# Performance work log

Hardware: AMD Instinct MI355X
Metric: run time of the kernel (lower is better)

Reference implementation:

```python
import jax, jax.numpy as jnp
import numpy as np

LN_EPS = 1e-5


def setup_inputs() -> dict:
    key = jax.random.key(0)
    k1, k2, k3, k4 = jax.random.split(key, 4)
    B, S, H, NH = 32, 256, 4096, 16
    scale = (2.0 ** 0.5) * ((3.0 / H) ** 0.5)
    inp = jax.random.normal(k1, (B, S, H), dtype=jnp.float32)
    mask = jax.random.randint(k2, (B, S), 0, 2, dtype=jnp.int32)  # 1 = padded key
    weight = jnp.ones((H,), dtype=jnp.float32)
    bias = jnp.zeros((H,), dtype=jnp.float32)
    qkv = jax.random.normal(k3, (H, 3 * H), dtype=jnp.float32) * scale
    o = jax.random.normal(k4, (H, H), dtype=jnp.float32) * scale
    return {"inp": inp, "mask": mask, "weight": weight, "bias": bias,
            "qkv": qkv, "o": o, "isPre": 1}


def _layer_norm(x, weight, bias):
    mu = jnp.mean(x, axis=-1, keepdims=True)
    var = jnp.mean(jnp.square(x - mu), axis=-1, keepdims=True)
    return (x - mu) * jax.lax.rsqrt(var + LN_EPS) * weight + bias


def _mha(x, mask, weight, bias, qkv, o, isPre, head_num=16):
    B, S, H = x.shape
    D = H // head_num
    xn = _layer_norm(x, weight, bias) if isPre else x
    # fused QKV projection: [B,S,3H]
    proj = jnp.einsum('bsh,hk->bsk', xn, qkv)
    q, k, v = jnp.split(proj, 3, axis=-1)
    q = q.reshape(B, S, head_num, D)
    k = k.reshape(B, S, head_num, D)
    v = v.reshape(B, S, head_num, D)
    scores = jnp.einsum('bqnd,bknd->bnqk', q, k) / jnp.sqrt(jnp.float32(D))
    # mask[b,k]==1 -> key k is padding, exclude from softmax
    neg = jnp.finfo(scores.dtype).min
    scores = jnp.where(mask[:, None, None, :] != 0, neg, scores)
    attn = jax.nn.softmax(scores, axis=-1)
    ctx = jnp.einsum('bnqk,bknd->bqnd', attn, v).reshape(B, S, H)
    out = jnp.einsum('bsh,ho->bso', ctx, o)
    if not isPre:
        out = _layer_norm(out, weight, bias)
    return out


def reference(inp, mask, weight, bias, qkv, o, isPre):
    return _mha(inp, mask, weight, bias, qkv, o, bool(isPre))
```

## Files before the change

kernel.cpp:

```cpp
#include <hip/hip_runtime.h>
#include <stdint.h>

typedef unsigned short u16;
typedef short bf16x8 __attribute__((ext_vector_type(8)));
typedef float f32x4 __attribute__((ext_vector_type(4)));

#define MFMA16(a, b, c) __builtin_amdgcn_mfma_f32_16x16x32_bf16((a), (b), (c), 0, 0, 0)

#define GLOAD_LDS16(gp, lp)                                                        \
  __builtin_amdgcn_global_load_lds((const __attribute__((address_space(1))) void*)(gp), \
                                   (__attribute__((address_space(3))) void*)(lp), 16, 0, 0)

#define BARRIER asm volatile("s_barrier" ::: "memory")
#define WAITV(n) asm volatile("s_waitcnt vmcnt(" #n ")" ::: "memory")

__device__ __forceinline__ u16 f2bf(float x) {
  union { float f; uint32_t u; } v; v.f = x;
  uint32_t r = (v.u + 0x7FFFu + ((v.u >> 16) & 1u)) >> 16;
  return (u16)r;
}

__global__ __launch_bounds__(256) void transpose_bf16(const float* __restrict__ in,
                                                      u16* __restrict__ out, int R, int C) {
  __shared__ float tile[32][33];
  int nCt = C >> 5;
  int bid = blockIdx.x;
  int r0 = (bid / nCt) << 5, c0 = (bid % nCt) << 5;
  int t = threadIdx.x;
  int r = t >> 3, cc = (t & 7) << 2;
  float4 v = *reinterpret_cast<const float4*>(in + (size_t)(r0 + r) * C + c0 + cc);
  tile[r][cc] = v.x; tile[r][cc + 1] = v.y; tile[r][cc + 2] = v.z; tile[r][cc + 3] = v.w;
  __syncthreads();
  int c = t >> 3, rr = (t & 7) << 2;
  ushort4 u;
  u.x = f2bf(tile[rr][c]);     u.y = f2bf(tile[rr + 1][c]);
  u.z = f2bf(tile[rr + 2][c]); u.w = f2bf(tile[rr + 3][c]);
  *reinterpret_cast<ushort4*>(out + (size_t)(c0 + c) * R + r0 + rr) = u;
}

__global__ __launch_bounds__(256) void ln_bf16(const float* __restrict__ in,
                                               const float* __restrict__ w,
                                               const float* __restrict__ bia,
                                               u16* __restrict__ out) {
  int row = blockIdx.x, t = threadIdx.x;
  const float* x = in + (size_t)row * 4096;
  float4 v[4];
  float s = 0.f, sq = 0.f;
#pragma unroll
  for (int i = 0; i < 4; i++) {
    v[i] = *reinterpret_cast<const float4*>(x + i * 1024 + t * 4);
    s  += v[i].x + v[i].y + v[i].z + v[i].w;
    sq += v[i].x * v[i].x + v[i].y * v[i].y + v[i].z * v[i].z + v[i].w * v[i].w;
  }
#pragma unroll
  for (int off = 32; off > 0; off >>= 1) { s += __shfl_down(s, off); sq += __shfl_down(sq, off); }
  __shared__ float red[8];
  int wid = t >> 6, lane = t & 63;
  if (lane == 0) { red[wid] = s; red[4 + wid] = sq; }
  __syncthreads();
  if (t == 0) {
    float st = red[0] + red[1] + red[2] + red[3];
    float sqt = red[4] + red[5] + red[6] + red[7];
    float mu = st * (1.f / 4096.f);
    float var = sqt * (1.f / 4096.f) - mu * mu;
    red[0] = mu; red[1] = rsqrtf(var + 1e-5f);
  }
  __syncthreads();
  float mu = red[0], rs = red[1];
#pragma unroll
  for (int i = 0; i < 4; i++) {
    float4 wv = *reinterpret_cast<const float4*>(w + i * 1024 + t * 4);
    float4 bv = *reinterpret_cast<const float4*>(bia + i * 1024 + t * 4);
    ushort4 u;
    u.x = f2bf((v[i].x - mu) * rs * wv.x + bv.x);
    u.y = f2bf((v[i].y - mu) * rs * wv.y + bv.y);
    u.z = f2bf((v[i].z - mu) * rs * wv.z + bv.z);
    u.w = f2bf((v[i].w - mu) * rs * wv.w + bv.w);
    *reinterpret_cast<ushort4*>(out + (size_t)row * 4096 + i * 1024 + t * 4) = u;
  }
}


#define LDA8(AR, Ab, mh) do {                                                     \
  _Pragma("unroll")                                                               \
  for (int mf = 0; mf < 4; mf++) {                                                \
    int lr = (mh)*128 + wm64 + mf*16 + llo;                                       \
    const char* rb = (Ab) + lr*128;                                               \
    int sw = (lr & 7) << 4;                                                       \
    AR[mf*2+0] = *reinterpret_cast<const bf16x8*>(rb + ((lhi16) ^ sw));           \
    AR[mf*2+1] = *reinterpret_cast<const bf16x8*>(rb + ((64 + lhi16) ^ sw));      \
  }                                                                               \
} while (0)

#define LDB4(BR, Bb, nh) do {                                                     \
  _Pragma("unroll")                                                               \
  for (int nf = 0; nf < 2; nf++) {                                                \
    int lr = (nh)*128 + wn32 + nf*16 + llo;                                       \
    const char* rb = (Bb) + lr*128;                                               \
    int sw = (lr & 7) << 4;                                                       \
    BR[nf*2+0] = *reinterpret_cast<const bf16x8*>(rb + ((lhi16) ^ sw));           \
    BR[nf*2+1] = *reinterpret_cast<const bf16x8*>(rb + ((64 + lhi16) ^ sw));      \
  }                                                                               \
} while (0)

#define MMAQ(AR, BR, mh, nh) do {                                                 \
  __builtin_amdgcn_s_setprio(1);                                                  \
  _Pragma("unroll")                                                               \
  for (int mf = 0; mf < 4; mf++)                                                  \
    _Pragma("unroll")                                                             \
    for (int nf = 0; nf < 2; nf++) {                                              \
      acc[(mh)*4+mf][(nh)*2+nf] = MFMA16(AR[mf*2+0], BR[nf*2+0], acc[(mh)*4+mf][(nh)*2+nf]); \
      acc[(mh)*4+mf][(nh)*2+nf] = MFMA16(AR[mf*2+1], BR[nf*2+1], acc[(mh)*4+mf][(nh)*2+nf]); \
    }                                                                             \
  __builtin_amdgcn_s_setprio(0);                                                  \
} while (0)

#define STAGE(isB, h, cbuf, ktile) do {                                           \
  const u16* g_ = (isB) ? Bt : A;                                                 \
  int base0_ = (isB) ? n0 : m0;                                                   \
  char* lb_ = smc + (cbuf)*65536 + (isB)*32768 + (h)*16384;                       \
  _Pragma("unroll")                                                               \
  for (int i_ = 0; i_ < 2; i_++) {                                                \
    int L_ = i_*512 + t;                                                          \
    int lr_ = (h)*128 + (L_ >> 3);                                                \
    int sl_ = (L_ & 7) ^ (lr_ & 7);                                               \
    int r_ = (isB) ? (((lr_ & 128) >> 2) | ((lr_ & 96) << 1) | (lr_ & 31))        \
                   : ((lr_ & 63) | ((lr_ & 64) << 1) | ((lr_ & 128) >> 1));       \
    GLOAD_LDS16(g_ + (size_t)(base0_ + r_) * K + (ktile)*64 + sl_*8, lb_ + L_*16);\
  }                                                                               \
} while (0)

template <int EPI>
__global__ __launch_bounds__(512, 2) void gemm256(const u16* __restrict__ A, const u16* __restrict__ Bt,
                                                  void* __restrict__ Cout, u16* __restrict__ vT,
                                                  int M, int N, int K, int nbn) {
  __shared__ u16 sm[65536];
  char* smc = (char*)sm;
  int bid = blockIdx.x;
  int s = bid >> 8, local = bid & 255;
  int xcd = local & 7, j = local >> 3;
  int trow = ((xcd >> 1) << 2) + (j >> 3);
  int tcol = ((xcd & 1) << 3) + (j & 7);
  int nsc = nbn >> 4;
  int sr = s / nsc, sc = s - sr * nsc;
  int tm = (sr << 4) + trow, tn = (sc << 4) + tcol;
  int m0 = tm << 8, n0 = tn << 8;
  int t = threadIdx.x;
  int w = t >> 6, lane = t & 63;
  int wm = w >> 2, wn = w & 3;
  int llo = lane & 15, lhi = lane >> 4;
  int wm64 = wm << 6, wn32 = wn << 5, lhi16 = lhi << 4;
  f32x4 acc[8][4] = {};
  bf16x8 aR[8], b0R[4], b1R[4];
  int NT = K >> 6;
  STAGE(0, 0, 0, 0); STAGE(1, 0, 0, 0); STAGE(1, 1, 0, 0); STAGE(0, 1, 0, 0);
  WAITV(4); BARRIER;
#pragma unroll 1
  for (int kt = 0; kt < NT - 1; kt++) {
    int c = kt & 1, cn = c ^ 1;
    const char* Ab = smc + c * 65536;
    const char* Bb = Ab + 32768;
    LDA8(aR, Ab, 0); LDB4(b0R, Bb, 0);
    STAGE(0, 0, cn, kt + 1);
    BARRIER;
    MMAQ(aR, b0R, 0, 0);
    WAITV(4); BARRIER;
    LDB4(b1R, Bb, 1);
    STAGE(1, 0, cn, kt + 1);
    BARRIER;
    MMAQ(aR, b1R, 0, 1);
    WAITV(4); BARRIER;
    LDA8(aR, Ab, 1);
    STAGE(1, 1, cn, kt + 1);
    BARRIER;
    MMAQ(aR, b1R, 1, 1);
    BARRIER;
    STAGE(0, 1, cn, kt + 1);
    BARRIER;
    MMAQ(aR, b0R, 1, 0);
    WAITV(4); BARRIER;
  }
  {
    int c = (NT - 1) & 1;
    const char* Ab = smc + c * 65536;
    const char* Bb = Ab + 32768;
    LDA8(aR, Ab, 0); LDB4(b0R, Bb, 0);
    MMAQ(aR, b0R, 0, 0);
    WAITV(2); BARRIER;
    LDB4(b1R, Bb, 1);
    MMAQ(aR, b1R, 0, 1);
    WAITV(0); BARRIER;
    LDA8(aR, Ab, 1);
    MMAQ(aR, b1R, 1, 1);
    MMAQ(aR, b0R, 1, 0);
  }
  if (EPI == 2) {
    float* C = (float*)Cout;
#pragma unroll
    for (int mi = 0; mi < 8; mi++)
#pragma unroll
      for (int ni = 0; ni < 4; ni++) {
        int m = m0 + wm * 128 + mi * 16 + lhi * 4;
        int n = n0 + wn * 64 + ni * 16 + llo;
#pragma unroll
        for (int r = 0; r < 4; r++) C[(size_t)(m + r) * N + n] = acc[mi][ni][r];
      }
  } else {
    if (n0 < 8192) {
      u16* qkb = (u16*)Cout;
#pragma unroll
      for (int mi = 0; mi < 8; mi++)
#pragma unroll
        for (int ni = 0; ni < 4; ni++) {
          int m = m0 + wm * 128 + mi * 16 + lhi * 4;
          int n = n0 + wn * 64 + ni * 16 + llo;
#pragma unroll
          for (int r = 0; r < 4; r++) qkb[(size_t)(m + r) * 8192 + n] = f2bf(acc[mi][ni][r]);
        }
    } else {
#pragma unroll
      for (int mi = 0; mi < 8; mi++)
#pragma unroll
        for (int ni = 0; ni < 4; ni++) {
          int m = m0 + wm * 128 + mi * 16 + lhi * 4;
          int n_ = n0 + wn * 64 + ni * 16 + llo - 8192;
          int h = n_ >> 8, d = n_ & 255;
          int b = m >> 8, s2 = m & 255;
          ushort4 u;
          u.x = f2bf(acc[mi][ni][0]); u.y = f2bf(acc[mi][ni][1]);
          u.z = f2bf(acc[mi][ni][2]); u.w = f2bf(acc[mi][ni][3]);
          *reinterpret_cast<ushort4*>(vT + ((size_t)((b << 4) + h) * 256 + d) * 256 + s2) = u;
        }
    }
  }
}

__global__ __launch_bounds__(256) void attn_kernel(const u16* __restrict__ qk,
                                                   const u16* __restrict__ vT,
                                                   const int* __restrict__ mask,
                                                   u16* __restrict__ ctx) {
  __shared__ u16 KV[64 * 256];
  __shared__ u16 P[64 * 256];
  __shared__ float maskf[256];
  int bx = blockIdx.x;
  int qt = bx & 3, h = (bx >> 2) & 15, b = bx >> 6;
  int t = threadIdx.x, wid = t >> 6, lane = t & 63, llo = lane & 15, lhi = lane >> 4;
  maskf[t] = mask[(b << 8) + t] ? -1e30f : 0.0f;
  bf16x8 qf[8];
  {
    const u16* qrow = qk + (size_t)((b << 8) + (qt << 6) + (wid << 4) + llo) * 8192 + (h << 8);
#pragma unroll
    for (int c = 0; c < 8; c++)
      qf[c] = *reinterpret_cast<const bf16x8*>(qrow + (lhi << 3) + (c << 5));
  }
  f32x4 sacc[16] = {};
#pragma unroll 1
  for (int kt = 0; kt < 4; kt++) {
    __syncthreads();
#pragma unroll
    for (int i = 0; i < 8; i++) {
      int G = (i << 8) + t;
      int key = G >> 5, g = G & 31;
      int gs = g ^ (key & 7);
      const u16* src = qk + (size_t)((b << 8) + (kt << 6) + key) * 8192 + 4096 + (h << 8) + (gs << 3);
      GLOAD_LDS16(src, (char*)KV + (G << 4));
    }
    __syncthreads();
#pragma unroll
    for (int nf = 0; nf < 4; nf++) {
      int kl = (nf << 4) + llo;
      const char* kb = (const char*)KV + (kl << 9);
      int sw = (kl & 7) << 4;
#pragma unroll
      for (int c = 0; c < 8; c++) {
        bf16x8 kf = *reinterpret_cast<const bf16x8*>(kb + (((lhi << 4) + (c << 6)) ^ sw));
        sacc[kt * 4 + nf] = MFMA16(qf[c], kf, sacc[kt * 4 + nf]);
      }
    }
  }
  float madd[16];
#pragma unroll
  for (int f = 0; f < 16; f++)
    madd[f] = maskf[((f >> 2) << 6) + ((f & 3) << 4) + llo];
  float mx[4] = {-3e38f, -3e38f, -3e38f, -3e38f};
#pragma unroll
  for (int f = 0; f < 16; f++)
#pragma unroll
    for (int r = 0; r < 4; r++) {
      float sv = sacc[f][r] * 0.0625f + madd[f];
      sacc[f][r] = sv;
      mx[r] = fmaxf(mx[r], sv);
    }
#pragma unroll
  for (int r = 0; r < 4; r++)
#pragma unroll
    for (int d = 1; d < 16; d <<= 1) mx[r] = fmaxf(mx[r], __shfl_xor(mx[r], d));
  float sum[4] = {0.f, 0.f, 0.f, 0.f};
#pragma unroll
  for (int f = 0; f < 16; f++)
#pragma unroll
    for (int r = 0; r < 4; r++) {
      float p = __expf(sacc[f][r] - mx[r]);
      sacc[f][r] = p;
      sum[r] += p;
    }
#pragma unroll
  for (int r = 0; r < 4; r++)
#pragma unroll
    for (int d = 1; d < 16; d <<= 1) sum[r] += __shfl_xor(sum[r], d);
  float rin[4];
#pragma unroll
  for (int r = 0; r < 4; r++) rin[r] = 1.f / sum[r];
#pragma unroll
  for (int r = 0; r < 4; r++) {
    int q = (wid << 4) + (lhi << 2) + r;
    char* pb = (char*)P + (q << 9);
    int sw = (q & 7) << 4;
#pragma unroll
    for (int f = 0; f < 16; f++) {
      int key = ((f >> 2) << 6) + ((f & 3) << 4) + llo;
      *reinterpret_cast<u16*>(pb + ((key << 1) ^ sw)) = f2bf(sacc[f][r] * rin[r]);
    }
  }
  f32x4 cacc[16] = {};
#pragma unroll 1
  for (int kt = 0; kt < 4; kt++) {
    __syncthreads();
#pragma unroll
    for (int i = 0; i < 8; i++) {
      int G = (i << 8) + t;
      int d = G >> 3, g = G & 7;
      int gs = g ^ (d & 7);
      const u16* src = vT + ((size_t)((b << 4) + h) * 256 + d) * 256 + (kt << 6) + (gs << 3);
      GLOAD_LDS16(src, (char*)KV + (G << 4));
    }
    __syncthreads();
    bf16x8 pf[2];
    {
      int q = (wid << 4) + llo;
      const char* pb = (const char*)P + (q << 9);
      int sw = (q & 7) << 4;
#pragma unroll
      for (int c = 0; c < 2; c++)
        pf[c] = *reinterpret_cast<const bf16x8*>(pb + (((kt << 7) + (c << 6) + (lhi << 4)) ^ sw));
    }
#pragma unroll
    for (int mf = 0; mf < 16; mf++) {
      int dl = (mf << 4) + llo;
      const char* vb = (const char*)KV + (dl << 7);
      int sw = (dl & 7) << 4;
#pragma unroll
      for (int c = 0; c < 2; c++) {
        bf16x8 vf = *reinterpret_cast<const bf16x8*>(vb + (((lhi << 4) + (c << 6)) ^ sw));
        cacc[mf] = MFMA16(vf, pf[c], cacc[mf]);
      }
    }
  }
  int token = (b << 8) + (qt << 6) + (wid << 4) + llo;
  u16* crow = ctx + (size_t)token * 4096 + (h << 8);
#pragma unroll
  for (int mf = 0; mf < 16; mf++) {
    ushort4 u;
    u.x = f2bf(cacc[mf][0]); u.y = f2bf(cacc[mf][1]);
    u.z = f2bf(cacc[mf][2]); u.w = f2bf(cacc[mf][3]);
    *reinterpret_cast<ushort4*>(crow + (mf << 4) + (lhi << 2)) = u;
  }
}

extern "C" void kernel_launch(void* const* d_in, const int* in_sizes, int n_in,
                              void* d_out, int out_size, void* d_ws, size_t ws_size,
                              hipStream_t stream) {
  const float* inp  = (const float*)d_in[0];
  const int*   mask = (const int*)d_in[1];
  const float* w    = (const float*)d_in[2];
  const float* bia  = (const float*)d_in[3];
  const float* qkvw = (const float*)d_in[4];
  const float* ow   = (const float*)d_in[5];
  const size_t MB = 1024ull * 1024ull;
  if (ws_size < 352 * MB) return;
  char* ws = (char*)d_ws;
  u16* xn   = (u16*)(ws);
  u16* qkvT = (u16*)(ws + 64 * MB);
  u16* qk   = (u16*)(ws + 160 * MB);
  u16* vT   = (u16*)(ws + 288 * MB);
  u16* oT   = (u16*)(ws + 64 * MB);
  u16* ctx  = (u16*)(ws);
  float* out = (float*)d_out;

  transpose_bf16<<<49152, 256, 0, stream>>>(qkvw, qkvT, 4096, 12288);
  ln_bf16<<<8192, 256, 0, stream>>>(inp, w, bia, xn);
  gemm256<1><<<1536, 512, 0, stream>>>(xn, qkvT, (void*)qk, vT, 8192, 12288, 4096, 48);
  transpose_bf16<<<16384, 256, 0, stream>>>(ow, oT, 4096, 4096);
  attn_kernel<<<2048, 256, 0, stream>>>(qk, vT, mask, ctx);
  gemm256<2><<<512, 512, 0, stream>>>(ctx, oT, (void*)out, nullptr, 8192, 4096, 4096, 16);
}
```

Baseline: 1.295 ms.

## Deepen GEMM LDS prefetch pipeline to stage quarter-tiles two k-steps ahead

Restructures the 256x256 bf16 GEMM main loop so that sub-tiles of the k+2 tile are loaded into the current buffer as soon as they have been consumed, in addition to prefetching the k+1 tile into the other buffer. The prologue now issues six stage loads and the vmcnt waits are relaxed, letting more global-to-LDS loads stay in flight while the MFMAs run. This is meant to hide more memory latency, at the cost of more complex buffer reuse ordering and a risk of races if a quarter is overwritten before every wave has read it.

```diff
diff --git a/kernel.cpp b/kernel.cpp
--- a/kernel.cpp
+++ b/kernel.cpp
@@ -128,6 +128,27 @@
                    : ((lr_ & 63) | ((lr_ & 64) << 1) | ((lr_ & 128) >> 1));       \
     GLOAD_LDS16(g_ + (size_t)(base0_ + r_) * K + (ktile)*64 + sl_*8, lb_ + L_*16);\
   }                                                                               \
+} while (0)
+
+#define TILE4(tt, S1, S2, W2, W4) do {                                            \
+  int c_ = (tt) & 1;                                                              \
+  const char* Ab = smc + c_ * 65536;                                              \
+  const char* Bb = Ab + 32768;                                                    \
+                                                                    \
+  LDA8(aR, Ab, 0); LDB4(b0R, Bb, 0);                                              \
+  if (S1) STAGE(1, 0, c_ ^ 1, (tt) + 1);                                          \
+  BARRIER; MMAQ(aR, b0R, 0, 0); BARRIER;                                          \
+                                                                    \
+  LDB4(b1R, Bb, 1);                                                               \
+  if (S1) STAGE(0, 1, c_ ^ 1, (tt) + 1);                                          \
+  BARRIER; MMAQ(aR, b1R, 0, 1); WAITV(W2); BARRIER;                               \
+                                                                    \
+  LDA8(aR, Ab, 1);                                                                \
+  if (S2) STAGE(0, 0, c_, (tt) + 2);                                              \
+  BARRIER; MMAQ(aR, b1R, 1, 1); BARRIER;                                          \
+                                                                    \
+  if (S2) STAGE(1, 1, c_, (tt) + 2);                                              \
+  BARRIER; MMAQ(aR, b0R, 1, 0); WAITV(W4); BARRIER;                               \
 } while (0)
 
 template <int EPI>
@@ -153,47 +174,13 @@
   f32x4 acc[8][4] = {};
   bf16x8 aR[8], b0R[4], b1R[4];
   int NT = K >> 6;
-  STAGE(0, 0, 0, 0); STAGE(1, 0, 0, 0); STAGE(1, 1, 0, 0); STAGE(0, 1, 0, 0);
-  WAITV(4); BARRIER;
+  STAGE(0, 0, 0, 0); STAGE(1, 1, 0, 0); STAGE(1, 0, 0, 0); STAGE(0, 1, 0, 0);
+  STAGE(0, 0, 1, 1); STAGE(1, 1, 1, 1);
+  WAITV(6); BARRIER;
 #pragma unroll 1
-  for (int kt = 0; kt < NT - 1; kt++) {
-    int c = kt & 1, cn = c ^ 1;
-    const char* Ab = smc + c * 65536;
-    const char* Bb = Ab + 32768;
-    LDA8(aR, Ab, 0); LDB4(b0R, Bb, 0);
-    STAGE(0, 0, cn, kt + 1);
-    BARRIER;
-    MMAQ(aR, b0R, 0, 0);
-    WAITV(4); BARRIER;
-    LDB4(b1R, Bb, 1);
-    STAGE(1, 0, cn, kt + 1);
-    BARRIER;
-    MMAQ(aR, b1R, 0, 1);
-    WAITV(4); BARRIER;
-    LDA8(aR, Ab, 1);
-    STAGE(1, 1, cn, kt + 1);
-    BARRIER;
-    MMAQ(aR, b1R, 1, 1);
-    BARRIER;
-    STAGE(0, 1, cn, kt + 1);
-    BARRIER;
-    MMAQ(aR, b0R, 1, 0);
-    WAITV(4); BARRIER;
-  }
-  {
-    int c = (NT - 1) & 1;
-    const char* Ab = smc + c * 65536;
-    const char* Bb = Ab + 32768;
-    LDA8(aR, Ab, 0); LDB4(b0R, Bb, 0);
-    MMAQ(aR, b0R, 0, 0);
-    WAITV(2); BARRIER;
-    LDB4(b1R, Bb, 1);
-    MMAQ(aR, b1R, 0, 1);
-    WAITV(0); BARRIER;
-    LDA8(aR, Ab, 1);
-    MMAQ(aR, b1R, 1, 1);
-    MMAQ(aR, b0R, 1, 0);
-  }
+  for (int tt = 0; tt < NT - 2; ++tt) TILE4(tt, 1, 1, 8, 6);
+  TILE4(NT - 2, 1, 0, 8, 2);
+  TILE4(NT - 1, 0, 0, 0, 0);
   if (EPI == 2) {
     float* C = (float*)Cout;
 #pragma unroll
```

New measurement: 1.297 ms. No clear change (+0.1%).
